# Optimization experiments

Measured on AMD Instinct MI355X. Metric: run time of the kernel, lower is better.

## Reference

```python
import jax, jax.numpy as jnp
import numpy as np
from jax import lax

G, N, S, K, R = 8, 4096, 2048, 64, 0.4   # graphs, nodes/graph, fps samples (ratio=0.5), max neighbors, radius
EPER = 65536                              # edges per graph (avg degree 16)
C = 13                                    # num_classes


def setup_inputs():
    key = jax.random.key(0)
    ks = jax.random.split(key, 8)
    norm = jax.random.normal(ks[0], (G * N, 3), jnp.float32)
    pos = jax.random.uniform(ks[1], (G * N, 3), jnp.float32)
    x = jax.random.normal(ks[2], (G * N, 2), jnp.float32)
    e = jax.random.randint(ks[3], (2, G, EPER), 0, N)
    off = (jnp.arange(G) * N)[None, :, None]
    edge_index = (e + off).reshape(2, G * EPER).astype(jnp.int64)
    batch = jnp.repeat(jnp.arange(G), N).astype(jnp.int64)
    def lin(k, i, o):
        return jax.random.normal(k, (i, o), jnp.float32) / np.float32(np.sqrt(i))
    W1 = lin(ks[4], 8, 64);    b1 = jnp.zeros((64,), jnp.float32)
    W2 = lin(ks[5], 72, 128);  b2 = jnp.zeros((128,), jnp.float32)
    W3 = lin(ks[6], 139, 256); b3 = jnp.zeros((256,), jnp.float32)
    lin_w = lin(ks[7], 256, C); lin_b = jnp.zeros((C,), jnp.float32)
    return dict(norm=norm, pos=pos, x=x, edge_index=edge_index, batch=batch,
                W1=W1, b1=b1, W2=W2, b2=b2, W3=W3, b3=b3, lin_w=lin_w, lin_b=lin_b)


def _gcn(h, src, dst, ew, W, b, n):
    # GCNConv(normalize=False): out[dst] += ew * (h @ W)[src]; + bias
    m = (h @ W)[src] * ew[:, None]
    return jax.ops.segment_sum(m, dst, num_segments=n) + b


def _fps(p):  # farthest point sampling on one graph, p: [N,3] -> [S] local indices (start at node 0)
    def step(carry, _):
        mind, cur = carry
        d = jnp.sum((p - p[cur]) ** 2, axis=1)
        mind = jnp.minimum(mind, d)
        return (mind, jnp.argmax(mind).astype(jnp.int32)), cur
    _, idx = lax.scan(step, (jnp.full((N,), jnp.inf, p.dtype), jnp.int32(0)), None, length=S)
    return idx


def _radius(p, q):  # p [N,3], q [S,3] -> neighbor cols [S,K] (lowest-index-first within radius), valid mask
    d2 = jnp.sum((q[:, None, :] - p[None, :, :]) ** 2, axis=-1)  # [S,N]
    mask = d2 < R * R
    score = jnp.where(mask, N - jnp.arange(N, dtype=jnp.int32)[None, :], 0)
    vals, cols = lax.top_k(score, K)
    valid = vals > 0
    return jnp.where(valid, cols, 0), valid


def reference(norm, pos, x, edge_index, batch, W1, b1, W2, b2, W3, b3, lin_w, lin_b):
    NT = G * N
    inp = jnp.concatenate([norm, pos, x], axis=1)          # [NT, 8]
    src, dst = edge_index[0], edge_index[1]
    ew = jnp.ones((src.shape[0],), inp.dtype)
    # dropout is inactive at inference (training=False)
    h1 = jax.nn.relu(_gcn(inp, src, dst, ew, W1, b1, NT))  # [NT, 64]
    h1 = jnp.concatenate([h1, inp], axis=1)                # [NT, 72]
    h2 = jax.nn.relu(_gcn(h1, src, dst, ew, W2, b2, NT))   # [NT, 128]

    pg = pos.reshape(G, N, 3)
    pgs = lax.stop_gradient(pg)
    idx_loc = jax.vmap(_fps)(pgs)                          # [G, S] local indices
    q = jax.vmap(lambda p, i: p[i])(pg, idx_loc)           # [G, S, 3] sampled positions
    cols, valid = jax.vmap(_radius)(pgs, lax.stop_gradient(q))  # [G, S, K]

    # PointConv with identity local_nn/global_nn: max over neighbors of [x_j, pos_j - pos_i]
    hg = h2.reshape(G, N, 128)
    def pconv(h, p, qv, c, v):
        msg = jnp.concatenate([h[c], p[c] - qv[:, None, :]], axis=-1)  # [S, K, 131]
        msg = jnp.where(v[..., None], msg, -jnp.inf)
        return jnp.max(msg, axis=1)                                    # [S, 131]
    x_int = jax.vmap(pconv)(hg, pg, q, cols, valid).reshape(G * S, 131)

    # filter_adj: keep edges with both endpoints sampled, remap to new ids
    idx_flat = (idx_loc + (jnp.arange(G) * N)[:, None]).reshape(-1)    # [G*S] global indices
    mapping = jnp.full((NT,), -1, jnp.int32).at[idx_flat].set(jnp.arange(G * S, dtype=jnp.int32))
    ns, nd = mapping[src], mapping[dst]
    em = (ns >= 0) & (nd >= 0)
    ew3 = em.astype(inp.dtype)
    ns = jnp.where(em, ns, 0)
    nd = jnp.where(em, nd, 0)

    h3in = jnp.concatenate([x_int, inp[idx_flat]], axis=1)  # [G*S, 139]
    h3 = jax.nn.relu(_gcn(h3in, ns, nd, ew3, W3, b3, G * S))  # [G*S, 256]

    pooled = h3.reshape(G, S, 256).max(axis=1)              # global_max_pool -> [G, 256]
    logits = pooled @ lin_w + lin_b
    out = jax.nn.log_softmax(logits, axis=1)
    pred = jax.nn.softmax(out, axis=1)
    return (out, pred)
```

## Files before the change

### kernel.cpp

```cpp
#include <hip/hip_runtime.h>
#include <hip/hip_bf16.h>

constexpr int NG   = 8;
constexpr int NPG  = 4096;
constexpr int NT   = NG * NPG;
constexpr int NS   = 2048;
constexpr int GS   = NG * NS;
constexpr int KN   = 64;
constexpr int NE   = NG * 65536;
constexpr int NC   = 13;
constexpr int NBW  = 504;

__device__ __forceinline__ float inp_val(const float* norm, const float* pos, const float* x,
                                         int node, int dim) {
  if (dim < 3) return norm[(size_t)node * 3 + dim];
  if (dim < 6) return pos[(size_t)node * 3 + (dim - 3)];
  return x[(size_t)node * 2 + (dim - 6)];
}

__global__ __launch_bounds__(256, 1) void phaseA_kernel(
    const float* __restrict__ pos, int* __restrict__ idxf, float* __restrict__ qpos,
    const float* __restrict__ norm, const float* __restrict__ x,
    const float* __restrict__ W1, float* __restrict__ t1,
    const int* __restrict__ ei, int* __restrict__ deg) {
  if (blockIdx.x >= 8) {
    int wb = blockIdx.x - 8;
    int sub = threadIdx.x >> 6;
    int f = threadIdx.x & 63;
    __shared__ float row[4][8];
    for (int n0 = wb * 4; n0 < NT; n0 += NBW * 4) {
      int n = n0 + sub;
      if (f < 8) row[sub][f] = inp_val(norm, pos, x, n, f);
      float acc = 0.f;
#pragma unroll
      for (int i = 0; i < 8; ++i) acc += row[sub][i] * W1[i * 64 + f];
      t1[(size_t)n * 64 + f] = acc;
    }
    for (int e = wb * 256 + threadIdx.x; e < NE; e += NBW * 256)
      atomicAdd(&deg[ei[NE + e]], 1);
    return;
  }
  const int g = blockIdx.x;
  __shared__ float4 sq[2][4];
  __shared__ int sidx[2][4];
  __shared__ float4 qrec[NS];
  __shared__ int irec[NS];
  const float* pg = pos + (size_t)g * NPG * 3;
  const int tid = threadIdx.x;
  const int wave = tid >> 6, lane = tid & 63;
  const int p0 = tid * 16;

  float a[48];
  {
    const float4* pg4 = reinterpret_cast<const float4*>(pg + (size_t)p0 * 3);
#pragma unroll
    for (int j = 0; j < 12; ++j) {
      float4 t = pg4[j];
      a[4 * j + 0] = t.x; a[4 * j + 1] = t.y; a[4 * j + 2] = t.z; a[4 * j + 3] = t.w;
    }
  }
  float px[16], py[16], pz[16], mind[16];
#pragma unroll
  for (int i = 0; i < 16; ++i) {
    px[i] = a[3 * i]; py[i] = a[3 * i + 1]; pz[i] = a[3 * i + 2];
    mind[i] = __int_as_float(0x7f800000);
  }
  float cx = pg[0], cy = pg[1], cz = pg[2];
  int idx_sel = 0;

  for (int s = 0; s < NS; ++s) {
    if (tid == 0) { irec[s] = idx_sel; qrec[s] = make_float4(cx, cy, cz, 0.f); }
    float bestv = -1.f, bx = 0.f, by = 0.f, bz = 0.f;
    int bi = 0;
#pragma unroll
    for (int i = 0; i < 16; ++i) {
      float dx = __fsub_rn(px[i], cx);
      float dy = __fsub_rn(py[i], cy);
      float dz = __fsub_rn(pz[i], cz);
      float dd = __fadd_rn(__fadd_rn(__fmul_rn(dx, dx), __fmul_rn(dy, dy)), __fmul_rn(dz, dz));
      float nm = fminf(mind[i], dd);
      mind[i] = nm;
      bool gt = nm > bestv;
      bestv = gt ? nm : bestv;
      bx = gt ? px[i] : bx;
      by = gt ? py[i] : by;
      bz = gt ? pz[i] : bz;
      bi = gt ? i : bi;
    }
    float v = bestv;
    v = fmaxf(v, __int_as_float(__builtin_amdgcn_update_dpp(0, __float_as_int(v), 0x111, 0xF, 0xF, true)));
    v = fmaxf(v, __int_as_float(__builtin_amdgcn_update_dpp(0, __float_as_int(v), 0x112, 0xF, 0xF, true)));
    v = fmaxf(v, __int_as_float(__builtin_amdgcn_update_dpp(0, __float_as_int(v), 0x114, 0xF, 0xF, true)));
    v = fmaxf(v, __int_as_float(__builtin_amdgcn_update_dpp(0, __float_as_int(v), 0x118, 0xF, 0xF, true)));
    v = fmaxf(v, __int_as_float(__builtin_amdgcn_update_dpp(0, __float_as_int(v), 0x142, 0xF, 0xF, true)));
    v = fmaxf(v, __int_as_float(__builtin_amdgcn_update_dpp(0, __float_as_int(v), 0x143, 0xF, 0xF, true)));
    int maxbits = __builtin_amdgcn_readlane(__float_as_int(v), 63);
    float wavemax = __int_as_float(maxbits);
    unsigned long long ball = __ballot(bestv == wavemax);
    int winner = __ffsll(ball) - 1;
    int b = s & 1;
    if (lane == winner) {
      sq[b][wave] = make_float4(bx, by, bz, wavemax);
      sidx[b][wave] = p0 + bi;
    }
    __syncthreads();
    float4 q0 = sq[b][0], q1 = sq[b][1], q2 = sq[b][2], q3 = sq[b][3];
    float4 qs = q3;
    if (q2.w >= qs.w) qs = q2;
    if (q1.w >= qs.w) qs = q1;
    if (q0.w >= qs.w) qs = q0;
    cx = qs.x; cy = qs.y; cz = qs.z;
    if (tid == 0) {
      int i0 = sidx[b][0], i1 = sidx[b][1], i2 = sidx[b][2], i3 = sidx[b][3];
      float r = q3.w; int is = i3;
      if (q2.w >= r) { r = q2.w; is = i2; }
      if (q1.w >= r) { r = q1.w; is = i1; }
      if (q0.w >= r) { r = q0.w; is = i0; }
      idx_sel = is;
    }
  }
  __syncthreads();
  for (int j = tid; j < NS; j += 256) {
    idxf[g * NS + j] = g * NPG + irec[j];
    float4 q = qrec[j];
    size_t m = (size_t)(g * NS + j) * 3;
    qpos[m + 0] = q.x; qpos[m + 1] = q.y; qpos[m + 2] = q.z;
  }
}

__global__ void feat2_kernel(const float* __restrict__ h1, const float* __restrict__ norm,
                             const float* __restrict__ pos, const float* __restrict__ x,
                             const float* __restrict__ W2, float* __restrict__ t2) {
  int n = blockIdx.x, f = threadIdx.x;
  __shared__ float row[72];
  if (f < 64) row[f] = h1[(size_t)n * 64 + f];
  else if (f < 72) row[f] = inp_val(norm, pos, x, n, f - 64);
  __syncthreads();
  float acc = 0.f;
#pragma unroll 8
  for (int i = 0; i < 72; ++i) acc += row[i] * W2[i * 128 + f];
  t2[(size_t)n * 128 + f] = acc;
}

__global__ void featdeg_kernel(const float* __restrict__ xint, const int* __restrict__ idxf,
                               const float* __restrict__ norm, const float* __restrict__ pos,
                               const float* __restrict__ x, const float* __restrict__ W3,
                               float* __restrict__ t3,
                               const int* __restrict__ ei, const int* __restrict__ mp,
                               int* __restrict__ deg) {
  if (blockIdx.x >= GS) {
    int e = (blockIdx.x - GS) * 256 + threadIdx.x;
    int ns = mp[ei[e]], nd = mp[ei[NE + e]];
    if (ns >= 0 && nd >= 0) atomicAdd(&deg[nd], 1);
    return;
  }
  int m = blockIdx.x, f = threadIdx.x;
  __shared__ float row[139];
  if (f < 131) row[f] = xint[(size_t)m * 131 + f];
  else if (f < 139) { int node = idxf[m]; row[f] = inp_val(norm, pos, x, node, f - 131); }
  __syncthreads();
  float acc = 0.f;
#pragma unroll 8
  for (int i = 0; i < 139; ++i) acc += row[i] * W3[i * 256 + f];
  t3[(size_t)m * 256 + f] = acc;
}

__global__ void fill1_kernel(const int* __restrict__ ei, const int* __restrict__ off,
                             int* __restrict__ cur, int* __restrict__ el) {
  int e = blockIdx.x * 256 + threadIdx.x;
  if (e < NE) {
    int sN = ei[e], dN = ei[NE + e];
    int p = off[dN] + atomicAdd(&cur[dN], 1);
    el[p] = sN;
  }
}

__global__ void fill2_kernel(const int* __restrict__ ei, const int* __restrict__ mp,
                             const int* __restrict__ off, int* __restrict__ cur,
                             int* __restrict__ el) {
  int e = blockIdx.x * 256 + threadIdx.x;
  if (e < NE) {
    int ns = mp[ei[e]], nd = mp[ei[NE + e]];
    if (ns >= 0 && nd >= 0) {
      int p = off[nd] + atomicAdd(&cur[nd], 1);
      el[p] = ns;
    }
  }
}

__global__ __launch_bounds__(1024) void scan_kernel(const int* __restrict__ in,
                                                    int* __restrict__ out, int n) {
  __shared__ int ls[1024];
  int tid = threadIdx.x;
  int per = (n + 1023) >> 10;
  int base = tid * per;
  int s = 0;
  for (int i = 0; i < per; ++i) { int idx = base + i; if (idx < n) s += in[idx]; }
  ls[tid] = s;
  __syncthreads();
  for (int d = 1; d < 1024; d <<= 1) {
    int v = (tid >= d) ? ls[tid - d] : 0;
    __syncthreads();
    ls[tid] += v;
    __syncthreads();
  }
  int excl = (tid == 0) ? 0 : ls[tid - 1];
  for (int i = 0; i < per; ++i) {
    int idx = base + i;
    if (idx < n) { out[idx] = excl; excl += in[idx]; }
  }
  if (tid == 1023) out[n] = ls[1023];
}

__global__ void agg_kernel(const float* __restrict__ t, const int* __restrict__ off,
                           const int* __restrict__ el, const float* __restrict__ b,
                           float* __restrict__ out, int F) {
  int node = blockIdx.x, f = threadIdx.x;
  int e0 = off[node], e1 = off[node + 1];
  float acc = 0.f;
  for (int j = e0; j < e1; ++j) acc += t[(size_t)el[j] * F + f];
  out[(size_t)node * F + f] = fmaxf(acc + b[f], 0.f);
}

__global__ __launch_bounds__(256) void radius_kernel(const float* __restrict__ pos,
                                                     const float* __restrict__ qpos,
                                                     int* __restrict__ cols,
                                                     int* __restrict__ cnt,
                                                     const int* __restrict__ idxf,
                                                     int* __restrict__ mp) {
  const int g = blockIdx.x;
  __shared__ float sx[NPG], sy[NPG], sz[NPG];
  const float* pg = pos + (size_t)g * NPG * 3;
  for (int i = threadIdx.x; i < NPG * 3; i += 256) {
    float v = pg[i]; int node = i / 3, c = i - node * 3;
    if (c == 0) sx[node] = v; else if (c == 1) sy[node] = v; else sz[node] = v;
  }
  __syncthreads();
  int m = g * NS + blockIdx.y * 256 + threadIdx.x;
  mp[idxf[m]] = m;
  float qx = qpos[(size_t)m * 3], qy = qpos[(size_t)m * 3 + 1], qz = qpos[(size_t)m * 3 + 2];
  int* out = cols + (size_t)m * KN;
  int c = 0;
  for (int i = 0; i < NPG; ++i) {
    float dx = __fsub_rn(sx[i], qx);
    float dy = __fsub_rn(sy[i], qy);
    float dz = __fsub_rn(sz[i], qz);
    float d2 = __fadd_rn(__fadd_rn(__fmul_rn(dx, dx), __fmul_rn(dy, dy)), __fmul_rn(dz, dz));
    if (d2 < 0.16f) {
      out[c++] = i;
      if (c == KN) break;
    }
  }
  cnt[m] = c;
}

__global__ __launch_bounds__(64) void pointconv_kernel(const float* __restrict__ h2,
                                                       const float* __restrict__ pos,
                                                       const float* __restrict__ qpos,
                                                       const int* __restrict__ cols,
                                                       const int* __restrict__ cnt,
                                                       float* __restrict__ xint) {
  int m = blockIdx.x, t = threadIdx.x;
  int g = m / NS;
  int n = cnt[m];
  const int* cl = cols + (size_t)m * KN;
  float m0 = -INFINITY, m1 = -INFINITY, mp = -INFINITY;
  for (int k = 0; k < n; ++k) {
    int c = cl[k];
    size_t base = (size_t)(g * NPG + c);
    m0 = fmaxf(m0, h2[base * 128 + t]);
    m1 = fmaxf(m1, h2[base * 128 + 64 + t]);
    if (t < 3) mp = fmaxf(mp, pos[base * 3 + t]);
  }
  float* xo = xint + (size_t)m * 131;
  xo[t] = m0;
  xo[64 + t] = m1;
  if (t < 3) xo[128 + t] = __fsub_rn(mp, qpos[(size_t)m * 3 + t]);
}

__global__ void pool_kernel(const float* __restrict__ h3, float* __restrict__ pooled) {
  int g = blockIdx.x, ch = blockIdx.y, f = threadIdx.x;
  float mx = 0.f;
  size_t base = ((size_t)g * NS + (size_t)ch * 256) * 256 + f;
  for (int s = 0; s < 256; ++s) mx = fmaxf(mx, h3[base + (size_t)s * 256]);
  atomicMax((int*)pooled + g * 256 + f, __float_as_int(mx));
}

__global__ void head_kernel(const float* __restrict__ pooled, const float* __restrict__ lw,
                            const float* __restrict__ lb, float* __restrict__ outp) {
  __shared__ float lg[NG * NC];
  int t = threadIdx.x;
  if (t < NG * NC) {
    int g = t / NC, c = t % NC;
    float acc = lb[c];
    for (int k = 0; k < 256; ++k) acc += pooled[g * 256 + k] * lw[k * NC + c];
    lg[t] = acc;
  }
  __syncthreads();
  if (t < NG) {
    int g = t;
    float mx = -INFINITY;
    for (int c = 0; c < NC; ++c) mx = fmaxf(mx, lg[g * NC + c]);
    float sum = 0.f;
    for (int c = 0; c < NC; ++c) sum += expf(lg[g * NC + c] - mx);
    float lse = logf(sum);
    float ov[NC];
    float mx2 = -INFINITY;
    for (int c = 0; c < NC; ++c) {
      ov[c] = lg[g * NC + c] - mx - lse;
      outp[g * NC + c] = ov[c];
      mx2 = fmaxf(mx2, ov[c]);
    }
    float s2 = 0.f;
    for (int c = 0; c < NC; ++c) s2 += expf(ov[c] - mx2);
    for (int c = 0; c < NC; ++c) outp[NG * NC + g * NC + c] = expf(ov[c] - mx2) / s2;
  }
}

extern "C" void kernel_launch(void* const* d_in, const int* in_sizes, int n_in,
                              void* d_out, int out_size, void* d_ws, size_t ws_size,
                              hipStream_t stream) {
  const float* norm = (const float*)d_in[0];
  const float* pos  = (const float*)d_in[1];
  const float* x    = (const float*)d_in[2];
  const int* ei     = (const int*)d_in[3];
  const float* W1 = (const float*)d_in[5];
  const float* b1 = (const float*)d_in[6];
  const float* W2 = (const float*)d_in[7];
  const float* b2 = (const float*)d_in[8];
  const float* W3 = (const float*)d_in[9];
  const float* b3 = (const float*)d_in[10];
  const float* lw = (const float*)d_in[11];
  const float* lb = (const float*)d_in[12];
  float* outp = (float*)d_out;

  char* w = (char*)d_ws;
  size_t o = 0;
  auto alloc = [&](size_t bytes) -> void* {
    void* p = w + o;
    o = (o + bytes + 255) & ~(size_t)255;
    return p;
  };
  float* A    = (float*)alloc((size_t)NT * 128 * 4);
  float* Bf   = (float*)alloc((size_t)NT * 128 * 4);
  float* xint = (float*)alloc((size_t)GS * 131 * 4);
  int* cols   = (int*)alloc((size_t)GS * KN * 4);
  int* cnt    = (int*)alloc((size_t)GS * 4);
  int* deg1   = (int*)alloc((size_t)NT * 4);
  int* off1   = (int*)alloc((size_t)(NT + 1) * 4);
  int* cur1   = (int*)alloc((size_t)NT * 4);
  int* el1    = (int*)alloc((size_t)NE * 4);
  int* deg2   = (int*)alloc((size_t)GS * 4);
  int* off2   = (int*)alloc((size_t)(GS + 1) * 4);
  int* cur2   = (int*)alloc((size_t)GS * 4);
  int* el2    = (int*)alloc((size_t)NE * 4);
  int* idxf   = (int*)alloc((size_t)GS * 4);
  float* qpos = (float*)alloc((size_t)GS * 3 * 4);
  int* mapv   = (int*)alloc((size_t)NT * 4);
  float* pooled = (float*)alloc((size_t)NG * 256 * 4);

  hipMemsetAsync(deg1, 0, (size_t)NT * 4, stream);
  hipMemsetAsync(cur1, 0, (size_t)NT * 4, stream);
  hipMemsetAsync(deg2, 0, (size_t)GS * 4, stream);
  hipMemsetAsync(cur2, 0, (size_t)GS * 4, stream);
  hipMemsetAsync(mapv, 0xFF, (size_t)NT * 4, stream);
  hipMemsetAsync(pooled, 0, (size_t)NG * 256 * 4, stream);

  phaseA_kernel<<<8 + NBW, 256, 0, stream>>>(pos, idxf, qpos, norm, x, W1, A, ei, deg1);
  scan_kernel<<<1, 1024, 0, stream>>>(deg1, off1, NT);
  fill1_kernel<<<NE / 256, 256, 0, stream>>>(ei, off1, cur1, el1);
  agg_kernel<<<NT, 64, 0, stream>>>(A, off1, el1, b1, Bf, 64);
  feat2_kernel<<<NT, 128, 0, stream>>>(Bf, norm, pos, x, W2, A);
  agg_kernel<<<NT, 128, 0, stream>>>(A, off1, el1, b2, Bf, 128);
  radius_kernel<<<dim3(NG, NS / 256), 256, 0, stream>>>(pos, qpos, cols, cnt, idxf, mapv);
  pointconv_kernel<<<GS, 64, 0, stream>>>(Bf, pos, qpos, cols, cnt, xint);
  featdeg_kernel<<<GS + NE / 256, 256, 0, stream>>>(xint, idxf, norm, pos, x, W3, A,
                                                    ei, mapv, deg2);
  scan_kernel<<<1, 1024, 0, stream>>>(deg2, off2, GS);
  fill2_kernel<<<NE / 256, 256, 0, stream>>>(ei, mapv, off2, cur2, el2);
  agg_kernel<<<GS, 256, 0, stream>>>(A, off2, el2, b3, Bf, 256);
  pool_kernel<<<dim3(NG, NS / 256), 256, 0, stream>>>(Bf, pooled);
  head_kernel<<<1, 128, 0, stream>>>(pooled, lw, lb, outp);
}
```

Baseline: 2.357 ms.

## Fuse GCN layers 1-2 into cooperative FPS kernel with grid barriers

Moves the degree scan, CSR fill, layer-1 aggregation, layer-2 feature transform and layer-2 aggregation into the worker blocks of the cooperative phaseA kernel. These stages run alongside the serial farthest-point-sampling blocks and are separated by atomic-counter grid barriers among the workers. This hides the GCN front half behind FPS and removes five launches. Layer-1 aggregation is also fused with the W2 matmul, so h1 is never written to memory. The cost is fewer worker blocks (248), a single-block serial scan, and the risk that spin barriers deadlock unless every block is co-resident.

```diff
diff --git a/kernel.cpp b/kernel.cpp
--- a/kernel.cpp
+++ b/kernel.cpp
@@ -9,7 +9,7 @@
 constexpr int KN   = 64;
 constexpr int NE   = NG * 65536;
 constexpr int NC   = 13;
-constexpr int NBW  = 504;
+constexpr int NWORK = 248;
 
 __device__ __forceinline__ float inp_val(const float* norm, const float* pos, const float* x,
                                          int node, int dim) {
@@ -18,26 +18,93 @@
   return x[(size_t)node * 2 + (dim - 6)];
 }
 
+__device__ __forceinline__ void wbar(int* ctrs, int k, int target) {
+  __syncthreads();
+  __threadfence();
+  if (threadIdx.x == 0) {
+    __hip_atomic_fetch_add(&ctrs[k], 1, __ATOMIC_RELEASE, __HIP_MEMORY_SCOPE_AGENT);
+    while (__hip_atomic_load(&ctrs[k], __ATOMIC_ACQUIRE, __HIP_MEMORY_SCOPE_AGENT) < target)
+      __builtin_amdgcn_s_sleep(16);
+  }
+  __syncthreads();
+}
+
 __global__ __launch_bounds__(256, 1) void phaseA_kernel(
     const float* __restrict__ pos, int* __restrict__ idxf, float* __restrict__ qpos,
     const float* __restrict__ norm, const float* __restrict__ x,
     const float* __restrict__ W1, float* __restrict__ t1,
-    const int* __restrict__ ei, int* __restrict__ deg) {
+    const int* __restrict__ ei, int* __restrict__ deg,
+    int* __restrict__ off1, int* __restrict__ cur1, int* __restrict__ el1,
+    const float* __restrict__ b1, const float* __restrict__ W2, float* __restrict__ t2,
+    const float* __restrict__ b2, float* __restrict__ h2,
+    int* __restrict__ wctr) {
   if (blockIdx.x >= 8) {
-    int wb = blockIdx.x - 8;
-    int sub = threadIdx.x >> 6;
-    int f = threadIdx.x & 63;
-    __shared__ float row[4][8];
-    for (int n0 = wb * 4; n0 < NT; n0 += NBW * 4) {
+    const int wb = blockIdx.x - 8;
+    const int sub = threadIdx.x >> 6;
+    const int f = threadIdx.x & 63;
+    __shared__ float wrow[4][80];
+    __shared__ int sscan[256];
+    for (int n0 = wb * 4; n0 < NT; n0 += NWORK * 4) {
       int n = n0 + sub;
-      if (f < 8) row[sub][f] = inp_val(norm, pos, x, n, f);
+      if (f < 8) wrow[sub][f] = inp_val(norm, pos, x, n, f);
       float acc = 0.f;
 #pragma unroll
-      for (int i = 0; i < 8; ++i) acc += row[sub][i] * W1[i * 64 + f];
+      for (int i = 0; i < 8; ++i) acc += wrow[sub][i] * W1[i * 64 + f];
       t1[(size_t)n * 64 + f] = acc;
     }
-    for (int e = wb * 256 + threadIdx.x; e < NE; e += NBW * 256)
+    for (int e = wb * 256 + threadIdx.x; e < NE; e += NWORK * 256)
       atomicAdd(&deg[ei[NE + e]], 1);
+    wbar(wctr, 0, NWORK);
+    if (wb == 0) {
+      int t = threadIdx.x, base = t * 128, s = 0;
+      for (int i = 0; i < 128; ++i) s += deg[base + i];
+      sscan[t] = s;
+      __syncthreads();
+      for (int d = 1; d < 256; d <<= 1) {
+        int v = (t >= d) ? sscan[t - d] : 0;
+        __syncthreads();
+        sscan[t] += v;
+        __syncthreads();
+      }
+      int excl = (t == 0) ? 0 : sscan[t - 1];
+      for (int i = 0; i < 128; ++i) { off1[base + i] = excl; excl += deg[base + i]; }
+      if (t == 255) off1[NT] = sscan[255];
+    }
+    wbar(wctr, 1, NWORK);
+    for (int e = wb * 256 + threadIdx.x; e < NE; e += NWORK * 256) {
+      int sN = ei[e], dN = ei[NE + e];
+      int p = off1[dN] + atomicAdd(&cur1[dN], 1);
+      el1[p] = sN;
+    }
+    wbar(wctr, 2, NWORK);
+    for (int n0 = wb * 4; n0 < NT; n0 += NWORK * 4) {
+      int n = n0 + sub;
+      int e0 = off1[n], e1 = off1[n + 1];
+      float acc = 0.f;
+      for (int j = e0; j < e1; ++j) acc += t1[(size_t)el1[j] * 64 + f];
+      wrow[sub][f] = fmaxf(acc + b1[f], 0.f);
+      if (f < 8) wrow[sub][64 + f] = inp_val(norm, pos, x, n, f);
+      float a0 = 0.f, a1 = 0.f;
+#pragma unroll 8
+      for (int i = 0; i < 72; ++i) {
+        float r = wrow[sub][i];
+        a0 += r * W2[i * 128 + f];
+        a1 += r * W2[i * 128 + 64 + f];
+      }
+      t2[(size_t)n * 128 + f] = a0;
+      t2[(size_t)n * 128 + 64 + f] = a1;
+    }
+    wbar(wctr, 3, NWORK);
+    {
+      const int f2 = threadIdx.x & 127, sub2 = threadIdx.x >> 7;
+      for (int n0 = wb * 2; n0 < NT; n0 += NWORK * 2) {
+        int n = n0 + sub2;
+        int e0 = off1[n], e1 = off1[n + 1];
+        float acc = 0.f;
+        for (int j = e0; j < e1; ++j) acc += t2[(size_t)el1[j] * 128 + f2];
+        h2[(size_t)n * 128 + f2] = fmaxf(acc + b2[f2], 0.f);
+      }
+    }
     return;
   }
   const int g = blockIdx.x;
@@ -128,20 +195,6 @@
   }
 }
 
-__global__ void feat2_kernel(const float* __restrict__ h1, const float* __restrict__ norm,
-                             const float* __restrict__ pos, const float* __restrict__ x,
-                             const float* __restrict__ W2, float* __restrict__ t2) {
-  int n = blockIdx.x, f = threadIdx.x;
-  __shared__ float row[72];
-  if (f < 64) row[f] = h1[(size_t)n * 64 + f];
-  else if (f < 72) row[f] = inp_val(norm, pos, x, n, f - 64);
-  __syncthreads();
-  float acc = 0.f;
-#pragma unroll 8
-  for (int i = 0; i < 72; ++i) acc += row[i] * W2[i * 128 + f];
-  t2[(size_t)n * 128 + f] = acc;
-}
-
 __global__ void featdeg_kernel(const float* __restrict__ xint, const int* __restrict__ idxf,
                                const float* __restrict__ norm, const float* __restrict__ pos,
                                const float* __restrict__ x, const float* __restrict__ W3,
@@ -163,16 +216,6 @@
 #pragma unroll 8
   for (int i = 0; i < 139; ++i) acc += row[i] * W3[i * 256 + f];
   t3[(size_t)m * 256 + f] = acc;
-}
-
-__global__ void fill1_kernel(const int* __restrict__ ei, const int* __restrict__ off,
-                             int* __restrict__ cur, int* __restrict__ el) {
-  int e = blockIdx.x * 256 + threadIdx.x;
-  if (e < NE) {
-    int sN = ei[e], dN = ei[NE + e];
-    int p = off[dN] + atomicAdd(&cur[dN], 1);
-    el[p] = sN;
-  }
 }
 
 __global__ void fill2_kernel(const int* __restrict__ ei, const int* __restrict__ mp,
@@ -343,6 +386,7 @@
   };
   float* A    = (float*)alloc((size_t)NT * 128 * 4);
   float* Bf   = (float*)alloc((size_t)NT * 128 * 4);
+  float* T1   = (float*)alloc((size_t)NT * 64 * 4);
   float* xint = (float*)alloc((size_t)GS * 131 * 4);
   int* cols   = (int*)alloc((size_t)GS * KN * 4);
   int* cnt    = (int*)alloc((size_t)GS * 4);
@@ -358,6 +402,7 @@
   float* qpos = (float*)alloc((size_t)GS * 3 * 4);
   int* mapv   = (int*)alloc((size_t)NT * 4);
   float* pooled = (float*)alloc((size_t)NG * 256 * 4);
+  int* wctr   = (int*)alloc(64);
 
   hipMemsetAsync(deg1, 0, (size_t)NT * 4, stream);
   hipMemsetAsync(cur1, 0, (size_t)NT * 4, stream);
@@ -365,13 +410,17 @@
   hipMemsetAsync(cur2, 0, (size_t)GS * 4, stream);
   hipMemsetAsync(mapv, 0xFF, (size_t)NT * 4, stream);
   hipMemsetAsync(pooled, 0, (size_t)NG * 256 * 4, stream);
-
-  phaseA_kernel<<<8 + NBW, 256, 0, stream>>>(pos, idxf, qpos, norm, x, W1, A, ei, deg1);
-  scan_kernel<<<1, 1024, 0, stream>>>(deg1, off1, NT);
-  fill1_kernel<<<NE / 256, 256, 0, stream>>>(ei, off1, cur1, el1);
-  agg_kernel<<<NT, 64, 0, stream>>>(A, off1, el1, b1, Bf, 64);
-  feat2_kernel<<<NT, 128, 0, stream>>>(Bf, norm, pos, x, W2, A);
-  agg_kernel<<<NT, 128, 0, stream>>>(A, off1, el1, b2, Bf, 128);
+  hipMemsetAsync(wctr, 0, 64, stream);
+
+  {
+    void* ka[] = {(void*)&pos, (void*)&idxf, (void*)&qpos, (void*)&norm, (void*)&x,
+                  (void*)&W1, (void*)&T1, (void*)&ei, (void*)&deg1,
+                  (void*)&off1, (void*)&cur1, (void*)&el1,
+                  (void*)&b1, (void*)&W2, (void*)&A, (void*)&b2, (void*)&Bf,
+                  (void*)&wctr};
+    hipLaunchCooperativeKernel((const void*)phaseA_kernel, dim3(8 + NWORK), dim3(256),
+                               ka, 0, stream);
+  }
   radius_kernel<<<dim3(NG, NS / 256), 256, 0, stream>>>(pos, qpos, cols, cnt, idxf, mapv);
   pointconv_kernel<<<GS, 64, 0, stream>>>(Bf, pos, qpos, cols, cnt, xint);
   featdeg_kernel<<<GS + NE / 256, 256, 0, stream>>>(xint, idxf, norm, pos, x, W3, A,
```

New measurement: 2.166 ms. -8.1%, faster.
